# Optimization experiments

Measured on AMD Instinct MI355X. Metric: run time of the kernel, lower is better.

The kernel has to match this reference:

```python
import jax, jax.numpy as jnp
import numpy as np

B, Hs, Ws, C = 4, 56, 56, 128
NH, K = 4, 7


def _layernorm(x, w, b, eps=1e-5):
    mu = jnp.mean(x, axis=-1, keepdims=True)
    var = jnp.mean((x - mu) ** 2, axis=-1, keepdims=True)
    return (x - mu) * jax.lax.rsqrt(var + eps) * w + b


def setup_inputs() -> dict:
    key = jax.random.key(0)
    ks = jax.random.split(key, 16)
    s = lambda k_, shape, fan: jax.random.normal(k_, shape, jnp.float32) * (fan ** -0.5)
    hid = 4 * C
    return {
        "x": jax.random.normal(ks[0], (B, Hs, Ws, C), jnp.float32),
        "norm1_w": jnp.ones((C,), jnp.float32),
        "norm1_b": jnp.zeros((C,), jnp.float32),
        "qkv_w": s(ks[1], (3 * C, C), C),
        "qkv_b": jnp.zeros((3 * C,), jnp.float32),
        "rpb": 0.02 * jax.random.normal(ks[2], (NH, 2 * K - 1, 2 * K - 1), jnp.float32),
        "proj_w": s(ks[3], (C, C), C),
        "proj_b": jnp.zeros((C,), jnp.float32),
        "norm2_w": jnp.ones((C,), jnp.float32),
        "norm2_b": jnp.zeros((C,), jnp.float32),
        "fc1_w": s(ks[4], (hid, C), C),
        "fc1_b": jnp.zeros((hid,), jnp.float32),
        "fc2_w": s(ks[5], (C, hid), hid),
        "fc2_b": jnp.zeros((C,), jnp.float32),
    }


def _neighborhood_attention(x, qkv_w, qkv_b, rpb, proj_w, proj_b):
    # x: [B, H, W, C]; NATTEN-style clamped sliding-window attention.
    b, h, w, c = x.shape
    nh = rpb.shape[0]
    k = (rpb.shape[1] + 1) // 2
    hd = c // nh
    scale = hd ** -0.5

    # static clamped window start indices (windows shifted to stay in-bounds)
    sh = np.clip(np.arange(h) - k // 2, 0, h - k)
    sw = np.clip(np.arange(w) - k // 2, 0, w - k)
    idx_h = sh[:, None] + np.arange(k)                  # [H, k]
    idx_w = sw[:, None] + np.arange(k)                  # [W, k]
    bias_h = idx_h - np.arange(h)[:, None] + (k - 1)    # [H, k] in [0, 2k-2]
    bias_w = idx_w - np.arange(w)[:, None] + (k - 1)    # [W, k]

    qkv = x @ qkv_w.T + qkv_b                           # [B,H,W,3C]
    qkv = qkv.reshape(b, h, w, 3, nh, hd)
    q = qkv[..., 0, :, :] * scale                       # [B,H,W,nh,hd]
    kk = qkv[..., 1, :, :]
    vv = qkv[..., 2, :, :]

    # gather neighborhood keys/values: [B,H,kh,W,kw,nh,hd]
    k_win = kk[:, idx_h][:, :, :, idx_w]
    v_win = vv[:, idx_h][:, :, :, idx_w]

    # attention scores + relative positional bias
    scores = jnp.einsum('bhwnd,bhiwjnd->bnhwij', q, k_win)   # [B,nh,H,W,kh,kw]
    bias = rpb[:, bias_h][:, :, :, bias_w]                   # [nh,H,kh,W,kw]
    bias = jnp.transpose(bias, (0, 1, 3, 2, 4))              # [nh,H,W,kh,kw]
    scores = scores + bias[None]

    attn = jax.nn.softmax(scores.reshape(b, nh, h, w, k * k), axis=-1)
    attn = attn.reshape(b, nh, h, w, k, k)
    out = jnp.einsum('bnhwij,bhiwjnd->bhwnd', attn, v_win)   # [B,H,W,nh,hd]
    out = out.reshape(b, h, w, c)
    return out @ proj_w.T + proj_b


def reference(x, norm1_w, norm1_b, qkv_w, qkv_b, rpb, proj_w, proj_b,
              norm2_w, norm2_b, fc1_w, fc1_b, fc2_w, fc2_b):
    # attention block (pre-norm, residual)
    y = _layernorm(x, norm1_w, norm1_b)
    y = _neighborhood_attention(y, qkv_w, qkv_b, rpb, proj_w, proj_b)
    x = x + y
    # MLP block
    z = _layernorm(x, norm2_w, norm2_b)
    z = jax.nn.gelu(z @ fc1_w.T + fc1_b, approximate=False)
    z = z @ fc2_w.T + fc2_b
    return x + z
```

## Files before the change

kernel.cpp:

```cpp
#include <hip/hip_runtime.h>
#include <math.h>

#define TOK 12544
#define CDIM 128
#define NHEAD 4
#define HD 32
#define KS 7
#define HSZ 56
#define WSZ 56

typedef __attribute__((ext_vector_type(8))) short short8;
typedef __attribute__((ext_vector_type(4))) float f32x4;

__device__ inline ushort f2b(float f) {
    uint u = __float_as_uint(f);
    u += 0x7fffu + ((u >> 16) & 1u);
    return (ushort)(u >> 16);
}

__global__ void convert_w(const float* __restrict__ a, const float* __restrict__ b,
                          const float* __restrict__ c, const float* __restrict__ d,
                          ushort* __restrict__ wb) {
    int e = (blockIdx.x * 256 + threadIdx.x) * 4;
    const float* src;
    if (e < 49152)       src = a + e;
    else if (e < 65536)  src = b + (e - 49152);
    else if (e < 131072) src = c + (e - 65536);
    else                 src = d + (e - 131072);
    float4 v = *(const float4*)src;
    uint2 pk;
    pk.x = (uint)f2b(v.x) | ((uint)f2b(v.y) << 16);
    pk.y = (uint)f2b(v.z) | ((uint)f2b(v.w) << 16);
    *(uint2*)(wb + e) = pk;
}

__device__ inline void ln_to_lds(const float* __restrict__ X, int m0,
                                 const float* __restrict__ lnw, const float* __restrict__ lnb,
                                 ushort* __restrict__ lds) {
    int wv = threadIdx.x >> 6, lane = threadIdx.x & 63;
    #pragma unroll
    for (int r = 0; r < 8; r++) {
        int rl = wv * 8 + r;
        float2 v = *(const float2*)(X + (size_t)(m0 + rl) * CDIM + lane * 2);
        float s = v.x + v.y;
        #pragma unroll
        for (int o = 32; o > 0; o >>= 1) s += __shfl_xor(s, o);
        float mu = s * (1.0f / 128.0f);
        float d0 = v.x - mu, d1 = v.y - mu;
        float sq = d0 * d0 + d1 * d1;
        #pragma unroll
        for (int o = 32; o > 0; o >>= 1) sq += __shfl_xor(sq, o);
        float rstd = rsqrtf(sq * (1.0f / 128.0f) + 1e-5f);
        float2 wv2 = *(const float2*)(lnw + lane * 2);
        float2 bv2 = *(const float2*)(lnb + lane * 2);
        uint pk = (uint)f2b(d0 * rstd * wv2.x + bv2.x)
                | ((uint)f2b(d1 * rstd * wv2.y + bv2.y) << 16);
        *(uint*)((char*)lds + rl * 256 + ((lane * 4) ^ ((rl & 7) << 4))) = pk;
    }
}

__global__ __launch_bounds__(512) void ln1_qkv(const float* __restrict__ X,
                                               const ushort* __restrict__ W,
                                               const float* __restrict__ bias,
                                               const float* __restrict__ lnw,
                                               const float* __restrict__ lnb,
                                               ushort* __restrict__ Y) {
    __shared__ ushort xn[64 * 128];
    int m0 = blockIdx.x * 64;
    ln_to_lds(X, m0, lnw, lnb, xn);
    __syncthreads();

    int wv = threadIdx.x >> 6, lane = threadIdx.x & 63;
    int lr = lane & 15, kg = lane >> 4;
    int n0 = wv * 48;
    f32x4 acc[4][3] = {};
    #pragma unroll
    for (int k0 = 0; k0 < 128; k0 += 32) {
        short8 bf[3];
        #pragma unroll
        for (int ni = 0; ni < 3; ni++)
            bf[ni] = *(const short8*)(W + (size_t)(n0 + ni * 16 + lr) * 128 + k0 + kg * 8);
        #pragma unroll
        for (int mg = 0; mg < 4; mg++) {
            int row = mg * 16 + lr;
            short8 a0 = *(const short8*)((char*)xn + row * 256 + ((k0 * 2 + kg * 16) ^ ((row & 7) << 4)));
            #pragma unroll
            for (int ni = 0; ni < 3; ni++)
                acc[mg][ni] = __builtin_amdgcn_mfma_f32_16x16x32_bf16(a0, bf[ni], acc[mg][ni], 0, 0, 0);
        }
    }
    #pragma unroll
    for (int mg = 0; mg < 4; mg++)
    #pragma unroll
    for (int ni = 0; ni < 3; ni++) {
        int base = n0 + ni * 16;
        int which = base >> 7;
        int rem   = base & 127;
        int head  = rem >> 5;
        int hd0   = rem & 31;
        float bn = bias[base + lr];
        float sc = (which == 0) ? 0.17677669529663687f : 1.0f;
        ushort* dst = Y + ((size_t)(which * 4 + head) * TOK) * HD + hd0 + lr;
        #pragma unroll
        for (int r = 0; r < 4; r++) {
            int row = m0 + mg * 16 + kg * 4 + r;
            float v = (acc[mg][ni][r] + bn) * sc;
            dst[(size_t)row * HD] = f2b(v);
        }
    }
}

__global__ __launch_bounds__(512) void proj_mlp(const ushort* __restrict__ aob,
                                                const ushort* __restrict__ Wp,
                                                const float* __restrict__ bp,
                                                const float* __restrict__ X,
                                                const ushort* __restrict__ W1,
                                                const float* __restrict__ b1,
                                                const ushort* __restrict__ W2,
                                                const float* __restrict__ b2,
                                                const float* __restrict__ lnw,
                                                const float* __restrict__ lnb,
                                                float* __restrict__ out) {
    __shared__ float  x2f[64 * 132];
    __shared__ ushort zn[64 * 128];
    __shared__ ushort hb[64 * 512];
    int m0 = blockIdx.x * 64;
    int wv = threadIdx.x >> 6, lane = threadIdx.x & 63;
    int lr = lane & 15, kg = lane >> 4;

    {
        int n0 = wv * 16;
        f32x4 accp[4] = {};
        #pragma unroll
        for (int k0 = 0; k0 < 128; k0 += 32) {
            short8 bf = *(const short8*)(Wp + (size_t)(n0 + lr) * 128 + k0 + kg * 8);
            #pragma unroll
            for (int mg = 0; mg < 4; mg++) {
                short8 a0 = *(const short8*)(aob + (size_t)(m0 + mg * 16 + lr) * 128 + k0 + kg * 8);
                accp[mg] = __builtin_amdgcn_mfma_f32_16x16x32_bf16(a0, bf, accp[mg], 0, 0, 0);
            }
        }
        float bn = bp[n0 + lr];
        #pragma unroll
        for (int mg = 0; mg < 4; mg++)
        #pragma unroll
        for (int r = 0; r < 4; r++) {
            int row = mg * 16 + kg * 4 + r;
            x2f[row * 132 + n0 + lr] = accp[mg][r] + bn
                                     + X[(size_t)(m0 + row) * CDIM + n0 + lr];
        }
    }
    __syncthreads();

    #pragma unroll
    for (int r = 0; r < 8; r++) {
        int rl = wv * 8 + r;
        float2 v = *(const float2*)&x2f[rl * 132 + lane * 2];
        float s = v.x + v.y;
        #pragma unroll
        for (int o = 32; o > 0; o >>= 1) s += __shfl_xor(s, o);
        float mu = s * (1.0f / 128.0f);
        float d0 = v.x - mu, d1 = v.y - mu;
        float sq = d0 * d0 + d1 * d1;
        #pragma unroll
        for (int o = 32; o > 0; o >>= 1) sq += __shfl_xor(sq, o);
        float rstd = rsqrtf(sq * (1.0f / 128.0f) + 1e-5f);
        float2 wv2 = *(const float2*)(lnw + lane * 2);
        float2 bv2 = *(const float2*)(lnb + lane * 2);
        uint pk = (uint)f2b(d0 * rstd * wv2.x + bv2.x)
                | ((uint)f2b(d1 * rstd * wv2.y + bv2.y) << 16);
        *(uint*)((char*)zn + rl * 256 + ((lane * 4) ^ ((rl & 7) << 4))) = pk;
    }
    __syncthreads();

    {
        f32x4 acc1[4][4] = {};
        int nc0 = wv * 64;
        #pragma unroll
        for (int k0 = 0; k0 < 128; k0 += 32) {
            short8 bf[4];
            #pragma unroll
            for (int ni = 0; ni < 4; ni++)
                bf[ni] = *(const short8*)(W1 + (size_t)(nc0 + ni * 16 + lr) * 128 + k0 + kg * 8);
            #pragma unroll
            for (int mg = 0; mg < 4; mg++) {
                int row = mg * 16 + lr;
                short8 a0 = *(const short8*)((char*)zn + row * 256 + ((k0 * 2 + kg * 16) ^ ((row & 7) << 4)));
                #pragma unroll
                for (int ni = 0; ni < 4; ni++)
                    acc1[mg][ni] = __builtin_amdgcn_mfma_f32_16x16x32_bf16(a0, bf[ni], acc1[mg][ni], 0, 0, 0);
            }
        }
        #pragma unroll
        for (int mg = 0; mg < 4; mg++)
        #pragma unroll
        for (int ni = 0; ni < 4; ni++) {
            int lc = nc0 + ni * 16 + lr;
            float bn = b1[lc];
            #pragma unroll
            for (int r = 0; r < 4; r++) {
                int row = mg * 16 + kg * 4 + r;
                float v = acc1[mg][ni][r] + bn;
                float t = v + 0.044715f * v * v * v;
                float sg = 1.0f / (1.0f + __expf(-1.5957691216f * t));
                v = v * sg;
                *(ushort*)((char*)hb + row * 1024 + ((lc * 2) ^ ((row & 7) << 4))) = f2b(v);
            }
        }
    }
    __syncthreads();

    int rw0 = (wv >> 2) * 32, cw0 = (wv & 3) * 32;
    f32x4 acc2[2][2] = {};
    #pragma unroll
    for (int k0 = 0; k0 < 512; k0 += 32) {
        short8 a0[2], bf[2];
        #pragma unroll
        for (int mi = 0; mi < 2; mi++) {
            int row = rw0 + mi * 16 + lr;
            a0[mi] = *(const short8*)((char*)hb + row * 1024 + ((k0 * 2 + kg * 16) ^ ((row & 7) << 4)));
        }
        #pragma unroll
        for (int ni = 0; ni < 2; ni++)
            bf[ni] = *(const short8*)(W2 + (size_t)(cw0 + ni * 16 + lr) * 512 + k0 + kg * 8);
        #pragma unroll
        for (int mi = 0; mi < 2; mi++)
        #pragma unroll
        for (int ni = 0; ni < 2; ni++)
            acc2[mi][ni] = __builtin_amdgcn_mfma_f32_16x16x32_bf16(a0[mi], bf[ni], acc2[mi][ni], 0, 0, 0);
    }

    #pragma unroll
    for (int mi = 0; mi < 2; mi++)
    #pragma unroll
    for (int ni = 0; ni < 2; ni++) {
        int col = cw0 + ni * 16 + lr;
        float bn = b2[col];
        #pragma unroll
        for (int r = 0; r < 4; r++) {
            int row = rw0 + mi * 16 + kg * 4 + r;
            out[(size_t)(m0 + row) * CDIM + col] = acc2[mi][ni][r] + bn + x2f[row * 132 + col];
        }
    }
}

__global__ __launch_bounds__(256) void nat_attn8(const ushort* __restrict__ qkv,
                                                 const float* __restrict__ rpb,
                                                 ushort* __restrict__ ao) {
    __shared__ ushort katt[8704];
    __shared__ ushort vs[32 * 232];
    __shared__ float rpl[169];
    ushort* ks = katt;

    int tid = threadIdx.x, wv = tid >> 6, lane = tid & 63;
    int lr = lane & 15, kg = lane >> 4;
    int bid = blockIdx.x;
    int blk = (bid & 7) * 98 + (bid >> 3);
    int tile = blk % 49, hb2 = blk / 49;
    int head = hb2 & 3, b = hb2 >> 2;
    int r0 = (tile / 7) * 8, c0 = (tile % 7) * 8;
    int hr0 = min(max(r0 - 3, 0), HSZ - 14);
    int hc0 = min(max(c0 - 3, 0), WSZ - 14);
    int bimg = b * HSZ * WSZ;

    const ushort* qb = qkv + (size_t)(0 + head) * TOK * HD;
    const ushort* kb = qkv + (size_t)(4 + head) * TOK * HD;
    const ushort* vb = qkv + (size_t)(8 + head) * TOK * HD;

    if (tid < 169) rpl[tid] = rpb[head * 169 + tid];
    for (int idx = tid; idx < 784; idx += 256) {
        int t = idx >> 2, c = idx & 3;
        int gtok = bimg + (hr0 + t / 14) * WSZ + hc0 + t % 14;
        short8 v = *(const short8*)(kb + (size_t)gtok * HD + c * 8);
        *(short8*)(ks + t * 32 + ((c ^ (t & 3)) << 3)) = v;
    }
    for (int idx = tid; idx < 392; idx += 256) {
        int pr = idx >> 2, c = idx & 3;
        int t = pr * 2;
        int gtok = bimg + (hr0 + t / 14) * WSZ + hc0 + t % 14;
        const ushort* vp = vb + (size_t)gtok * HD + c * 8;
        short8 v0 = *(const short8*)vp;
        short8 v1 = *(const short8*)(vp + HD);
        #pragma unroll
        for (int q = 0; q < 8; q++)
            *(uint*)(vs + (c * 8 + q) * 232 + t) =
                (uint)(ushort)v0[q] | ((uint)(ushort)v1[q] << 16);
    }
    for (int idx = tid; idx < 32 * 18; idx += 256)
        *(uint*)(vs + (idx / 18) * 232 + 196 + (idx % 18) * 2) = 0;
    __syncthreads();

    int i0 = r0 + 2 * wv;
    int hw0 = min(max(i0 - 3, 0), HSZ - KS);
    int dwr = hw0 - hr0;
    int tbase = dwr * 14;
    int rb = tbase & ~7;
    int rboff = tbase - rb;

    int lpix = lr;
    int agp = bimg + (r0 + 2 * wv + (lpix >> 3)) * WSZ + c0 + (lpix & 7);
    short8 aq = *(const short8*)(qb + (size_t)agp * HD + kg * 8);
    f32x4 sc[7];
    #pragma unroll
    for (int tl = 0; tl < 7; tl++) {
        int t = tbase + tl * 16 + lr;
        short8 bk = *(const short8*)(ks + t * 32 + ((kg ^ (t & 3)) << 3));
        f32x4 z = {0.f, 0.f, 0.f, 0.f};
        sc[tl] = __builtin_amdgcn_mfma_f32_16x16x32_bf16(aq, bk, z, 0, 0, 0);
    }
    __syncthreads();

    ushort* attw = katt + wv * 16 * 136;
    #pragma unroll
    for (int z = 0; z < 2; z++) {
        int ii = z * 64 + lane;
        int row = ii >> 3, c2 = (ii & 7) * 2;
        int col = c2 + (c2 < rboff ? 0 : 112);
        *(uint*)(attw + row * 136 + col) = 0;
    }

    float inv[4];
    #pragma unroll
    for (int r = 0; r < 4; r++) {
        int idx = kg * 4 + r;
        int i = r0 + 2 * wv + (idx >> 3), j = c0 + (idx & 7);
        int shh = min(max(i - 3, 0), HSZ - KS);
        int sww = min(max(j - 3, 0), WSZ - KS);
        int dih = shh - hr0, dj = sww - hc0;
        int offh = hr0 - i + 6, offw = hc0 - j + 6;
        float sum = 0.f;
        #pragma unroll
        for (int tl = 0; tl < 7; tl++) {
            int t = tbase + tl * 16 + lr;
            int thr = (unsigned)t / 14u;
            int twr = t - thr * 14;
            bool in = ((unsigned)(thr - dih) < 7u) && ((unsigned)(twr - dj) < 7u);
            int bidx = (thr + offh) * 13 + (twr + offw);
            bidx = min(max(bidx, 0), 168);
            float e = in ? __expf(sc[tl][r] + rpl[bidx]) : 0.f;
            sum += e;
            attw[idx * 136 + rboff + tl * 16 + lr] = f2b(e);
        }
        #pragma unroll
        for (int o = 8; o > 0; o >>= 1) sum += __shfl_xor(sum, o);
        inv[r] = 1.0f / sum;
    }

    f32x4 po[2] = {};
    #pragma unroll
    for (int kst = 0; kst < 4; kst++) {
        short8 pa = *(const short8*)(attw + lr * 136 + kst * 32 + kg * 8);
        #pragma unroll
        for (int n = 0; n < 2; n++) {
            short8 vbf = *(const short8*)(vs + (n * 16 + lr) * 232 + rb + kst * 32 + kg * 8);
            po[n] = __builtin_amdgcn_mfma_f32_16x16x32_bf16(pa, vbf, po[n], 0, 0, 0);
        }
    }

    #pragma unroll
    for (int n = 0; n < 2; n++)
    #pragma unroll
    for (int rr = 0; rr < 4; rr++) {
        int idx = kg * 4 + rr;
        int gp = bimg + (r0 + 2 * wv + (idx >> 3)) * WSZ + c0 + (idx & 7);
        ao[(size_t)gp * CDIM + head * HD + n * 16 + lr] = f2b(po[n][rr] * inv[rr]);
    }
}

extern "C" void kernel_launch(void* const* d_in, const int* in_sizes, int n_in,
                              void* d_out, int out_size, void* d_ws, size_t ws_size,
                              hipStream_t stream) {
    const float* x      = (const float*)d_in[0];
    const float* n1w    = (const float*)d_in[1];
    const float* n1b    = (const float*)d_in[2];
    const float* qkv_w  = (const float*)d_in[3];
    const float* qkv_b  = (const float*)d_in[4];
    const float* rpb    = (const float*)d_in[5];
    const float* proj_w = (const float*)d_in[6];
    const float* proj_b = (const float*)d_in[7];
    const float* n2w    = (const float*)d_in[8];
    const float* n2b    = (const float*)d_in[9];
    const float* fc1_w  = (const float*)d_in[10];
    const float* fc1_b  = (const float*)d_in[11];
    const float* fc2_w  = (const float*)d_in[12];
    const float* fc2_b  = (const float*)d_in[13];
    float* out = (float*)d_out;

    ushort* wb   = (ushort*)d_ws;
    ushort* qkvb = wb + 196608;
    ushort* aob  = qkvb + (size_t)TOK * 384;

    const ushort* w_qkv  = wb;
    const ushort* w_proj = wb + 49152;
    const ushort* w_fc1  = wb + 65536;
    const ushort* w_fc2  = wb + 131072;

    convert_w<<<192, 256, 0, stream>>>(qkv_w, proj_w, fc1_w, fc2_w, wb);
    ln1_qkv<<<TOK / 64, 512, 0, stream>>>(x, w_qkv, qkv_b, n1w, n1b, qkvb);
    nat_attn8<<<4 * NHEAD * 49, 256, 0, stream>>>(qkvb, rpb, aob);
    proj_mlp<<<TOK / 64, 512, 0, stream>>>(aob, w_proj, proj_b, x,
                                           w_fc1, fc1_b, w_fc2, fc2_b, n2w, n2b, out);
}
```

Before: 58.54 us.

## Pre-swizzle bf16 weights into MFMA fragment order and fuse layernorm reductions

The weight conversion kernel now writes the bf16 weights in MFMA B-fragment order, grouped by 16 output rows, k-step and k-group. Each lane's 16-byte weight load in the GEMMs becomes part of a contiguous wave-wide read instead of a strided row access. Both layernorms now reduce sum and sum of squares in one shuffle loop rather than two sequential reductions. The single-pass E[x^2]-mu^2 variance is numerically less robust than the two-pass form.

```diff
diff --git a/kernel.cpp b/kernel.cpp
--- a/kernel.cpp
+++ b/kernel.cpp
@@ -12,26 +12,39 @@
 typedef __attribute__((ext_vector_type(8))) short short8;
 typedef __attribute__((ext_vector_type(4))) float f32x4;
 
-__device__ inline ushort f2b(float f) {
+__device__ inline uint f2b(float f) {
     uint u = __float_as_uint(f);
     u += 0x7fffu + ((u >> 16) & 1u);
-    return (ushort)(u >> 16);
-}
+    return u >> 16;
+}
+__device__ inline float b2f(ushort u) { return __uint_as_float((uint)u << 16); }
 
 __global__ void convert_w(const float* __restrict__ a, const float* __restrict__ b,
                           const float* __restrict__ c, const float* __restrict__ d,
                           ushort* __restrict__ wb) {
-    int e = (blockIdx.x * 256 + threadIdx.x) * 4;
-    const float* src;
-    if (e < 49152)       src = a + e;
-    else if (e < 65536)  src = b + (e - 49152);
-    else if (e < 131072) src = c + (e - 65536);
-    else                 src = d + (e - 131072);
-    float4 v = *(const float4*)src;
-    uint2 pk;
-    pk.x = (uint)f2b(v.x) | ((uint)f2b(v.y) << 16);
-    pk.y = (uint)f2b(v.z) | ((uint)f2b(v.w) << 16);
-    *(uint2*)(wb + e) = pk;
+    int u = blockIdx.x * 256 + threadIdx.x;
+    int e = u * 8;
+    const float* src; int base, K;
+    if (e < 49152)       { src = a; base = 0;      K = 128; }
+    else if (e < 65536)  { src = b; base = 49152;  K = 128; }
+    else if (e < 131072) { src = c; base = 65536;  K = 128; }
+    else                 { src = d; base = 131072; K = 512; }
+    int lu = (e - base) >> 3;
+    int lr = lu & 15;
+    int t  = lu >> 4;
+    int kg = t & 3; t >>= 2;
+    int kk32 = K >> 5;
+    int k0g = t % kk32;
+    int ngrp = t / kk32;
+    const float* s = src + (size_t)(ngrp * 16 + lr) * K + k0g * 32 + kg * 8;
+    float4 v0 = *(const float4*)s;
+    float4 v1 = *(const float4*)(s + 4);
+    uint4 pk;
+    pk.x = f2b(v0.x) | (f2b(v0.y) << 16);
+    pk.y = f2b(v0.z) | (f2b(v0.w) << 16);
+    pk.z = f2b(v1.x) | (f2b(v1.y) << 16);
+    pk.w = f2b(v1.z) | (f2b(v1.w) << 16);
+    *(uint4*)(wb + base + (size_t)lu * 8) = pk;
 }
 
 __device__ inline void ln_to_lds(const float* __restrict__ X, int m0,
@@ -42,19 +55,21 @@
     for (int r = 0; r < 8; r++) {
         int rl = wv * 8 + r;
         float2 v = *(const float2*)(X + (size_t)(m0 + rl) * CDIM + lane * 2);
-        float s = v.x + v.y;
-        #pragma unroll
-        for (int o = 32; o > 0; o >>= 1) s += __shfl_xor(s, o);
+        float s  = v.x + v.y;
+        float s2 = v.x * v.x + v.y * v.y;
+        #pragma unroll
+        for (int o = 32; o > 0; o >>= 1) {
+            s  += __shfl_xor(s, o);
+            s2 += __shfl_xor(s2, o);
+        }
         float mu = s * (1.0f / 128.0f);
+        float var = s2 * (1.0f / 128.0f) - mu * mu;
+        float rstd = rsqrtf(var + 1e-5f);
         float d0 = v.x - mu, d1 = v.y - mu;
-        float sq = d0 * d0 + d1 * d1;
-        #pragma unroll
-        for (int o = 32; o > 0; o >>= 1) sq += __shfl_xor(sq, o);
-        float rstd = rsqrtf(sq * (1.0f / 128.0f) + 1e-5f);
         float2 wv2 = *(const float2*)(lnw + lane * 2);
         float2 bv2 = *(const float2*)(lnb + lane * 2);
-        uint pk = (uint)f2b(d0 * rstd * wv2.x + bv2.x)
-                | ((uint)f2b(d1 * rstd * wv2.y + bv2.y) << 16);
+        uint pk = f2b(d0 * rstd * wv2.x + bv2.x)
+                | (f2b(d1 * rstd * wv2.y + bv2.y) << 16);
         *(uint*)((char*)lds + rl * 256 + ((lane * 4) ^ ((rl & 7) << 4))) = pk;
     }
 }
@@ -79,7 +94,7 @@
         short8 bf[3];
         #pragma unroll
         for (int ni = 0; ni < 3; ni++)
-            bf[ni] = *(const short8*)(W + (size_t)(n0 + ni * 16 + lr) * 128 + k0 + kg * 8);
+            bf[ni] = *(const short8*)(W + (size_t)(((((wv * 3 + ni) * 4 + (k0 >> 5)) * 4 + kg) * 16 + lr)) * 8);
         #pragma unroll
         for (int mg = 0; mg < 4; mg++) {
             int row = mg * 16 + lr;
@@ -105,7 +120,7 @@
         for (int r = 0; r < 4; r++) {
             int row = m0 + mg * 16 + kg * 4 + r;
             float v = (acc[mg][ni][r] + bn) * sc;
-            dst[(size_t)row * HD] = f2b(v);
+            dst[(size_t)row * HD] = (ushort)f2b(v);
         }
     }
 }
@@ -133,7 +148,7 @@
         f32x4 accp[4] = {};
         #pragma unroll
         for (int k0 = 0; k0 < 128; k0 += 32) {
-            short8 bf = *(const short8*)(Wp + (size_t)(n0 + lr) * 128 + k0 + kg * 8);
+            short8 bf = *(const short8*)(Wp + (size_t)((((wv * 4 + (k0 >> 5)) * 4 + kg) * 16 + lr)) * 8);
             #pragma unroll
             for (int mg = 0; mg < 4; mg++) {
                 short8 a0 = *(const short8*)(aob + (size_t)(m0 + mg * 16 + lr) * 128 + k0 + kg * 8);
@@ -156,19 +171,21 @@
     for (int r = 0; r < 8; r++) {
         int rl = wv * 8 + r;
         float2 v = *(const float2*)&x2f[rl * 132 + lane * 2];
-        float s = v.x + v.y;
-        #pragma unroll
-        for (int o = 32; o > 0; o >>= 1) s += __shfl_xor(s, o);
+        float s  = v.x + v.y;
+        float s2 = v.x * v.x + v.y * v.y;
+        #pragma unroll
+        for (int o = 32; o > 0; o >>= 1) {
+            s  += __shfl_xor(s, o);
+            s2 += __shfl_xor(s2, o);
+        }
         float mu = s * (1.0f / 128.0f);
+        float var = s2 * (1.0f / 128.0f) - mu * mu;
+        float rstd = rsqrtf(var + 1e-5f);
         float d0 = v.x - mu, d1 = v.y - mu;
-        float sq = d0 * d0 + d1 * d1;
-        #pragma unroll
-        for (int o = 32; o > 0; o >>= 1) sq += __shfl_xor(sq, o);
-        float rstd = rsqrtf(sq * (1.0f / 128.0f) + 1e-5f);
         float2 wv2 = *(const float2*)(lnw + lane * 2);
         float2 bv2 = *(const float2*)(lnb + lane * 2);
-        uint pk = (uint)f2b(d0 * rstd * wv2.x + bv2.x)
-                | ((uint)f2b(d1 * rstd * wv2.y + bv2.y) << 16);
+        uint pk = f2b(d0 * rstd * wv2.x + bv2.x)
+                | (f2b(d1 * rstd * wv2.y + bv2.y) << 16);
         *(uint*)((char*)zn + rl * 256 + ((lane * 4) ^ ((rl & 7) << 4))) = pk;
     }
     __syncthreads();
@@ -181,7 +198,7 @@
             short8 bf[4];
             #pragma unroll
             for (int ni = 0; ni < 4; ni++)
-                bf[ni] = *(const short8*)(W1 + (size_t)(nc0 + ni * 16 + lr) * 128 + k0 + kg * 8);
+                bf[ni] = *(const short8*)(W1 + (size_t)(((((wv * 4 + ni) * 4 + (k0 >> 5)) * 4 + kg) * 16 + lr)) * 8);
             #pragma unroll
             for (int mg = 0; mg < 4; mg++) {
                 int row = mg * 16 + lr;
@@ -204,7 +221,7 @@
                 float t = v + 0.044715f * v * v * v;
                 float sg = 1.0f / (1.0f + __expf(-1.5957691216f * t));
                 v = v * sg;
-                *(ushort*)((char*)hb + row * 1024 + ((lc * 2) ^ ((row & 7) << 4))) = f2b(v);
+                *(ushort*)((char*)hb + row * 1024 + ((lc * 2) ^ ((row & 7) << 4))) = (ushort)f2b(v);
             }
         }
     }
@@ -222,7 +239,7 @@
         }
         #pragma unroll
         for (int ni = 0; ni < 2; ni++)
-            bf[ni] = *(const short8*)(W2 + (size_t)(cw0 + ni * 16 + lr) * 512 + k0 + kg * 8);
+            bf[ni] = *(const short8*)(W2 + (size_t)((((((wv & 3) * 2 + ni) * 16 + (k0 >> 5)) * 4 + kg) * 16 + lr)) * 8);
         #pragma unroll
         for (int mi = 0; mi < 2; mi++)
         #pragma unroll
@@ -339,7 +356,7 @@
             bidx = min(max(bidx, 0), 168);
             float e = in ? __expf(sc[tl][r] + rpl[bidx]) : 0.f;
             sum += e;
-            attw[idx * 136 + rboff + tl * 16 + lr] = f2b(e);
+            attw[idx * 136 + rboff + tl * 16 + lr] = (ushort)f2b(e);
         }
         #pragma unroll
         for (int o = 8; o > 0; o >>= 1) sum += __shfl_xor(sum, o);
@@ -363,7 +380,7 @@
     for (int rr = 0; rr < 4; rr++) {
         int idx = kg * 4 + rr;
         int gp = bimg + (r0 + 2 * wv + (idx >> 3)) * WSZ + c0 + (idx & 7);
-        ao[(size_t)gp * CDIM + head * HD + n * 16 + lr] = f2b(po[n][rr] * inv[rr]);
+        ao[(size_t)gp * CDIM + head * HD + n * 16 + lr] = (ushort)f2b(po[n][rr] * inv[rr]);
     }
 }
 
@@ -395,7 +412,7 @@
     const ushort* w_fc1  = wb + 65536;
     const ushort* w_fc2  = wb + 131072;
 
-    convert_w<<<192, 256, 0, stream>>>(qkv_w, proj_w, fc1_w, fc2_w, wb);
+    convert_w<<<96, 256, 0, stream>>>(qkv_w, proj_w, fc1_w, fc2_w, wb);
     ln1_qkv<<<TOK / 64, 512, 0, stream>>>(x, w_qkv, qkv_b, n1w, n1b, qkvb);
     nat_attn8<<<4 * NHEAD * 49, 256, 0, stream>>>(qkvb, rpb, aob);
     proj_mlp<<<TOK / 64, 512, 0, stream>>>(aob, w_proj, proj_b, x,
```

New measurement: 52.41 us. 1.12x faster.
